# Kernel optimization log

Hardware: AMD Instinct MI355X
Metric: run time of the kernel (lower is better)

## Reference

```python
import jax, jax.numpy as jnp
import numpy as np

B, N, C, H, NUM, K = 4, 4096, 256, 512, 4, 10
GS1 = H // NUM   # feature-group size = 128
GS2 = N // NUM   # point-group size  = 1024


def _mlp2(x, w1, b1, w2, b2):
    # Linear -> ReLU -> Linear
    return jax.nn.relu(x @ w1 + b1) @ w2 + b2


def setup_inputs() -> dict:
    key = jax.random.key(0)
    ks = jax.random.split(key, 32)
    s = 0.02
    def w(i, shape):
        return jax.random.normal(ks[i], shape, dtype=jnp.float32) * s
    return {
        "features": jax.random.normal(ks[0], (B, C, N), dtype=jnp.float32),
        "xyz": jax.random.uniform(ks[1], (B, N, 3), dtype=jnp.float32),
        # fc1 / fc2 (stored [in,out] for x @ W)
        "fc1_w": w(2, (C, H)), "fc1_b": jnp.zeros((H,), jnp.float32),
        "fc2_w": w(3, (H, C)), "fc2_b": jnp.zeros((C,), jnp.float32),
        # fc_delta: Linear(3,H) -> ReLU -> Linear(H,H)
        "fd1_w": w(4, (3, H)), "fd1_b": jnp.zeros((H,), jnp.float32),
        "fd2_w": w(5, (H, H)), "fd2_b": jnp.zeros((H,), jnp.float32),
        # fc_gamma: Linear(H,H) -> ReLU -> Linear(H,H)
        "fg1_w": w(6, (H, H)), "fg1_b": jnp.zeros((H,), jnp.float32),
        "fg2_w": w(7, (H, H)), "fg2_b": jnp.zeros((H,), jnp.float32),
        # fc_gamma_2: Linear(GS1,GS1) -> ReLU -> Linear(GS1,GS1)
        "fgh1_w": w(8, (GS1, GS1)), "fgh1_b": jnp.zeros((GS1,), jnp.float32),
        "fgh2_w": w(9, (GS1, GS1)), "fgh2_b": jnp.zeros((GS1,), jnp.float32),
        # projections (no bias)
        "wqs": w(10, (H, H)), "wks": w(11, (H, H)), "wvs": w(12, (H, H)),
        "wqs2": w(13, (GS1, GS1)), "wks2": w(14, (GS1, GS1)),
    }


def reference(features, xyz, fc1_w, fc1_b, fc2_w, fc2_b, fd1_w, fd1_b, fd2_w, fd2_b,
              fg1_w, fg1_b, fg2_w, fg2_b, fgh1_w, fgh1_b, fgh2_w, fgh2_b,
              wqs, wks, wvs, wqs2, wks2):
    pre = features                                  # [B, C, N]
    x = jnp.swapaxes(features, 1, 2) @ fc1_w + fc1_b  # [B, N, H]

    # ---- attn1: feature-group subtraction attention (shared small weights per group)
    xg = x.reshape(B, N, NUM, GS1)
    q1 = jnp.einsum('bngc,cd->bngd', xg, wqs2)
    k1 = jnp.einsum('bngc,cd->bngd', xg, wks2)
    a1 = _mlp2(q1 - k1, fgh1_w, fgh1_b, fgh2_w, fgh2_b)
    a1 = jax.nn.softmax(a1 / np.sqrt(GS1).astype(np.float32), axis=1)  # softmax over points
    attn1 = a1.reshape(B, N, H)

    # ---- attn2: point-group attention. NOTE: source loop reuses stale index `i`
    # (== NUM-1) so every group is computed from the LAST point group; we replicate that.
    gf2 = x[:, (NUM - 1) * GS2:NUM * GS2, :]        # [B, GS2, H]
    q2 = gf2 @ wqs
    k2 = gf2 @ wks
    a2 = _mlp2(q2 - k2, fg1_w, fg1_b, fg2_w, fg2_b)
    a2 = jax.nn.softmax(a2 / np.sqrt(H).astype(np.float32), axis=-2)
    attn2 = jnp.tile(a2, (1, NUM, 1))               # [B, N, H]

    attn = attn1 + attn2
    v = x @ wvs                                     # [B, N, H]

    # ---- KNN positional encoding
    # square_distance
    d = (jnp.sum(xyz ** 2, -1)[:, :, None] + jnp.sum(xyz ** 2, -1)[:, None, :]
         - 2.0 * jnp.einsum('bnd,bmd->bnm', xyz, xyz))  # [B, N, N]
    knn_idx = jax.lax.top_k(-d, K)[1]               # [B, N, K] smallest distances
    knn_xyz = jax.vmap(lambda pts, idx: pts[idx])(xyz, knn_idx)  # [B, N, K, 3]
    pos_enc = _mlp2(xyz[:, :, None, :] - knn_xyz, fd1_w, fd1_b, fd2_w, fd2_b)  # [B,N,K,H]
    pos_enc = pos_enc.mean(axis=2)                  # [B, N, H]

    res = attn * (v + pos_enc)                      # einsum('bmf,bmf->bmf')
    new_features = jnp.swapaxes(res @ fc2_w + fc2_b, 1, 2) + pre  # [B, C, N]
    return (new_features, xyz)
```

## Files before the change

kernel.cpp:

```cpp
#include <hip/hip_runtime.h>
#include <cstdio>

typedef long long ll;
typedef unsigned long long ull;
typedef unsigned short ushort_t;
typedef __bf16 bf16x8 __attribute__((ext_vector_type(8)));
typedef float f32x4 __attribute__((ext_vector_type(4)));
typedef float f32x2 __attribute__((ext_vector_type(2)));

#define BB 4
#define NN 4096
#define CC 256
#define HH 512
#define GNUM 4
#define GS1 128
#define KNN 10

#define SC1 0.08838834764831845f
#define SC2 0.044194173824159216f

#define OFF_FC1T   0
#define OFF_WD2T   131072
#define OFF_FGH1T  147456
#define OFF_FGH2T  163840
#define OFF_WDT    180224
#define OFF_FG1T   442368
#define OFF_FG2T   704512
#define OFF_WVST   966656
#define OFF_FD2T   1228800
#define OFF_FC2T   1490944
#define WT_TOTAL   1622016

__device__ inline unsigned pk2(float x, float y) {
  unsigned a = __float_as_uint(x), b = __float_as_uint(y);
  a = (a + 0x7FFFu + ((a >> 16) & 1u)) >> 16;
  b = (b + 0x7FFFu + ((b >> 16) & 1u)) >> 16;
  return a | (b << 16);
}
__device__ inline ushort_t bf1(float x) {
  unsigned a = __float_as_uint(x);
  return (ushort_t)((a + 0x7FFFu + ((a >> 16) & 1u)) >> 16);
}
__device__ inline float b2f(ushort_t u) { return __uint_as_float((unsigned)u << 16); }
__device__ inline int sw16(int r) { return ((r ^ (r >> 3)) & 7) << 4; }

__device__ inline void xcd_map(int& bx, int& by, int& bz) {
  const int nx = gridDim.x, ny = gridDim.y;
  const int nwg = nx * ny * gridDim.z;
  const int bidf = blockIdx.x + nx * (blockIdx.y + ny * blockIdx.z);
  const int lid = (bidf & 7) * (nwg >> 3) + (bidf >> 3);
  bx = lid % nx;
  const int rem = lid / nx;
  by = rem % ny;
  bz = rem / ny;
}

__global__ __launch_bounds__(256) void wconv_k(
    const float* __restrict__ fc1w, const float* __restrict__ wqs2, const float* __restrict__ wks2,
    const float* __restrict__ fgh1, const float* __restrict__ fgh2,
    const float* __restrict__ wqs, const float* __restrict__ wks,
    const float* __restrict__ fg1, const float* __restrict__ fg2,
    const float* __restrict__ wvs, const float* __restrict__ fd2,
    const float* __restrict__ fc2w, ushort_t* __restrict__ WT)
{
  const int gc = blockIdx.x * 256 + threadIdx.x;
  const int e0 = gc * 8;
  if (e0 >= WT_TOTAL) return;
  const float* src = nullptr; const float* src2 = nullptr;
  int off, Kd, Nd;
  if (e0 < OFF_WD2T)        { src = fc1w;             off = OFF_FC1T;  Kd = 256; Nd = 512; }
  else if (e0 < OFF_FGH1T)  { src = wqs2; src2 = wks2; off = OFF_WD2T;  Kd = 128; Nd = 128; }
  else if (e0 < OFF_FGH2T)  { src = fgh1;             off = OFF_FGH1T; Kd = 128; Nd = 128; }
  else if (e0 < OFF_WDT)    { src = fgh2;             off = OFF_FGH2T; Kd = 128; Nd = 128; }
  else if (e0 < OFF_FG1T)   { src = wqs;  src2 = wks;  off = OFF_WDT;   Kd = 512; Nd = 512; }
  else if (e0 < OFF_FG2T)   { src = fg1;              off = OFF_FG1T;  Kd = 512; Nd = 512; }
  else if (e0 < OFF_WVST)   { src = fg2;              off = OFF_FG2T;  Kd = 512; Nd = 512; }
  else if (e0 < OFF_FD2T)   { src = wvs;              off = OFF_WVST;  Kd = 512; Nd = 512; }
  else if (e0 < OFF_FC2T)   { src = fd2;              off = OFF_FD2T;  Kd = 512; Nd = 512; }
  else                      { src = fc2w;             off = OFF_FC2T;  Kd = 512; Nd = 256; }
  const int local = e0 - off;
  const int n = local / Kd, k0 = local % Kd;
  ushort_t outv[8];
  #pragma unroll
  for (int j = 0; j < 8; ++j) {
    float v = src[(ll)(k0 + j) * Nd + n];
    if (src2) v -= src2[(ll)(k0 + j) * Nd + n];
    outv[j] = bf1(v);
  }
  *reinterpret_cast<uint4*>(WT + e0) = *reinterpret_cast<uint4*>(outv);
}

template<bool ATRANS, int EPI>
__global__ __launch_bounds__(256, 2) void mgemm_k(
    const void* __restrict__ Ain, const ushort_t* __restrict__ BT,
    const float* __restrict__ bias, void* __restrict__ CoutV,
    const float* __restrict__ pre,
    int M, int N, int K, int lda, ll strideA, ll strideC)
{
  int bx, by, z;
  xcd_map(bx, by, z);
  const int bm = by * 128;
  const int bn = bx * 128;
  __shared__ alignas(16) char smem[32768];
  char* smA = smem;
  char* smB = smem + 16384;
  const int tid = threadIdx.x;
  const int lane = tid & 63, w = tid >> 6;
  const int lr = lane & 15, lg = lane >> 4;
  const int wm = (w & 1) * 64, wn = (w >> 1) * 64;

  const ushort_t* Ab = ATRANS ? nullptr : ((const ushort_t*)Ain + (ll)z * strideA);
  const float*    Af = ATRANS ? ((const float*)Ain + (ll)z * strideA) : nullptr;

  f32x4 acc[4][4] = {};

  for (int k0 = 0; k0 < K; k0 += 64) {
    if (!ATRANS) {
      #pragma unroll
      for (int p = 0; p < 4; ++p) {
        const int i = p * 256 + tid;
        const int r = i >> 3, c8 = (i & 7) * 8;
        const uint4 v = *reinterpret_cast<const uint4*>(Ab + (ll)(bm + r) * lda + (k0 + c8));
        *reinterpret_cast<uint4*>(smA + r * 128 + ((c8 * 2) ^ sw16(r))) = v;
      }
    } else {
      #pragma unroll
      for (int p = 0; p < 2; ++p) {
        const int bb = p * 256 + tid;
        const int mb = (bb & 31) * 4, kb = (bb >> 5) * 4;
        const float4 l0 = *reinterpret_cast<const float4*>(Af + (ll)(k0 + kb + 0) * lda + (bm + mb));
        const float4 l1 = *reinterpret_cast<const float4*>(Af + (ll)(k0 + kb + 1) * lda + (bm + mb));
        const float4 l2 = *reinterpret_cast<const float4*>(Af + (ll)(k0 + kb + 2) * lda + (bm + mb));
        const float4 l3 = *reinterpret_cast<const float4*>(Af + (ll)(k0 + kb + 3) * lda + (bm + mb));
        *reinterpret_cast<uint2*>(smA + (mb + 0) * 128 + ((kb * 2) ^ sw16(mb + 0))) = make_uint2(pk2(l0.x, l1.x), pk2(l2.x, l3.x));
        *reinterpret_cast<uint2*>(smA + (mb + 1) * 128 + ((kb * 2) ^ sw16(mb + 1))) = make_uint2(pk2(l0.y, l1.y), pk2(l2.y, l3.y));
        *reinterpret_cast<uint2*>(smA + (mb + 2) * 128 + ((kb * 2) ^ sw16(mb + 2))) = make_uint2(pk2(l0.z, l1.z), pk2(l2.z, l3.z));
        *reinterpret_cast<uint2*>(smA + (mb + 3) * 128 + ((kb * 2) ^ sw16(mb + 3))) = make_uint2(pk2(l0.w, l1.w), pk2(l2.w, l3.w));
      }
    }
    #pragma unroll
    for (int p = 0; p < 4; ++p) {
      const int i = p * 256 + tid;
      const int r = i >> 3, c8 = (i & 7) * 8;
      const uint4 v = *reinterpret_cast<const uint4*>(BT + (ll)(bn + r) * K + (k0 + c8));
      *reinterpret_cast<uint4*>(smB + r * 128 + ((c8 * 2) ^ sw16(r))) = v;
    }
    __syncthreads();

    #pragma unroll
    for (int ks = 0; ks < 2; ++ks) {
      bf16x8 af[4], bfr[4];
      #pragma unroll
      for (int mi = 0; mi < 4; ++mi) {
        const int r = wm + mi * 16 + lr;
        af[mi] = *reinterpret_cast<const bf16x8*>(smA + r * 128 + ((((ks << 2) + lg) << 4) ^ sw16(r)));
      }
      #pragma unroll
      for (int ni = 0; ni < 4; ++ni) {
        const int r = wn + ni * 16 + lr;
        bfr[ni] = *reinterpret_cast<const bf16x8*>(smB + r * 128 + ((((ks << 2) + lg) << 4) ^ sw16(r)));
      }
      #pragma unroll
      for (int mi = 0; mi < 4; ++mi)
        #pragma unroll
        for (int ni = 0; ni < 4; ++ni)
          acc[mi][ni] = __builtin_amdgcn_mfma_f32_16x16x32_bf16(af[mi], bfr[ni], acc[mi][ni], 0, 0, 0);
    }
    __syncthreads();
  }

  #pragma unroll
  for (int ni = 0; ni < 4; ++ni) {
    const int col = bn + wn + ni * 16 + lr;
    const float bv = (EPI != 0) ? bias[col] : 0.f;
    #pragma unroll
    for (int mi = 0; mi < 4; ++mi) {
      const int row0 = bm + wm + mi * 16 + lg * 4;
      if (EPI == 4) {
        float* Cout = (float*)CoutV;
        const size_t o = ((size_t)z * N + col) * (size_t)M + row0;
        const float4 pv = *reinterpret_cast<const float4*>(pre + o);
        float4 r;
        r.x = acc[mi][ni][0] + bv + pv.x;
        r.y = acc[mi][ni][1] + bv + pv.y;
        r.z = acc[mi][ni][2] + bv + pv.z;
        r.w = acc[mi][ni][3] + bv + pv.w;
        *reinterpret_cast<float4*>(Cout + o) = r;
      } else {
        ushort_t* Co = (ushort_t*)CoutV + (ll)z * strideC;
        #pragma unroll
        for (int i = 0; i < 4; ++i) {
          float val = acc[mi][ni][i] + bv;
          if (EPI == 2) val = fmaxf(val, 0.f);
          Co[(ll)(row0 + i) * N + col] = bf1(val);
        }
      }
    }
  }
}

__global__ __launch_bounds__(256, 2) void gemm_vpe_k(
    const ushort_t* __restrict__ X, const ushort_t* __restrict__ HM,
    const ushort_t* __restrict__ wvT, const ushort_t* __restrict__ w2T,
    const float* __restrict__ bias, ushort_t* __restrict__ Cout)
{
  int bx, by, z;
  xcd_map(bx, by, z);
  const int bm = by * 128;
  const int bn = bx * 128;
  __shared__ alignas(16) char smem[32768];
  char* smA = smem;
  char* smB = smem + 16384;
  const int tid = threadIdx.x;
  const int lane = tid & 63, w = tid >> 6;
  const int lr = lane & 15, lg = lane >> 4;
  const int wm = (w & 1) * 64, wn = (w >> 1) * 64;

  f32x4 acc[4][4] = {};

  for (int k0 = 0; k0 < 1024; k0 += 64) {
    const ushort_t* A = (k0 < 512) ? X : HM;
    const ushort_t* BT = (k0 < 512) ? wvT : w2T;
    const int kk = k0 & 511;
    #pragma unroll
    for (int p = 0; p < 4; ++p) {
      const int i = p * 256 + tid;
      const int r = i >> 3, c8 = (i & 7) * 8;
      const uint4 v = *reinterpret_cast<const uint4*>(A + (ll)(bm + r) * 512 + (kk + c8));
      *reinterpret_cast<uint4*>(smA + r * 128 + ((c8 * 2) ^ sw16(r))) = v;
    }
    #pragma unroll
    for (int p = 0; p < 4; ++p) {
      const int i = p * 256 + tid;
      const int r = i >> 3, c8 = (i & 7) * 8;
      const uint4 v = *reinterpret_cast<const uint4*>(BT + (ll)(bn + r) * 512 + (kk + c8));
      *reinterpret_cast<uint4*>(smB + r * 128 + ((c8 * 2) ^ sw16(r))) = v;
    }
    __syncthreads();

    #pragma unroll
    for (int ks = 0; ks < 2; ++ks) {
      bf16x8 af[4], bfr[4];
      #pragma unroll
      for (int mi = 0; mi < 4; ++mi) {
        const int r = wm + mi * 16 + lr;
        af[mi] = *reinterpret_cast<const bf16x8*>(smA + r * 128 + ((((ks << 2) + lg) << 4) ^ sw16(r)));
      }
      #pragma unroll
      for (int ni = 0; ni < 4; ++ni) {
        const int r = wn + ni * 16 + lr;
        bfr[ni] = *reinterpret_cast<const bf16x8*>(smB + r * 128 + ((((ks << 2) + lg) << 4) ^ sw16(r)));
      }
      #pragma unroll
      for (int mi = 0; mi < 4; ++mi)
        #pragma unroll
        for (int ni = 0; ni < 4; ++ni)
          acc[mi][ni] = __builtin_amdgcn_mfma_f32_16x16x32_bf16(af[mi], bfr[ni], acc[mi][ni], 0, 0, 0);
    }
    __syncthreads();
  }

  #pragma unroll
  for (int ni = 0; ni < 4; ++ni) {
    const int col = bn + wn + ni * 16 + lr;
    const float bv = bias[col];
    #pragma unroll
    for (int mi = 0; mi < 4; ++mi) {
      const int row0 = bm + wm + mi * 16 + lg * 4;
      #pragma unroll
      for (int i = 0; i < 4; ++i)
        Cout[(ll)(row0 + i) * 512 + col] = bf1(acc[mi][ni][i] + bv);
    }
  }
}

__device__ __forceinline__ void gemm128(const char* smA, const char* smW, int wrow, int lr, int lg,
                                        f32x4 acc[8]) {
  #pragma unroll
  for (int ks = 0; ks < 4; ++ks) {
    const int koff = (ks * 4 + lg) * 16;
    const int ra = wrow + lr;
    const bf16x8 a = *reinterpret_cast<const bf16x8*>(smA + ra * 256 + (koff ^ sw16(ra)));
    #pragma unroll
    for (int ni = 0; ni < 8; ++ni) {
      const int rn = ni * 16 + lr;
      const bf16x8 b = *reinterpret_cast<const bf16x8*>(smW + rn * 256 + (koff ^ sw16(rn)));
      acc[ni] = __builtin_amdgcn_mfma_f32_16x16x32_bf16(a, b, acc[ni], 0, 0, 0);
    }
  }
}

__device__ __forceinline__ void stageWTb(const ushort_t* __restrict__ W, char* smW, int tid) {
  #pragma unroll
  for (int p = 0; p < 4; ++p) {
    const int i = p * 512 + tid;
    const int r = i >> 4, c8 = (i & 15) * 8;
    const uint4 v = *reinterpret_cast<const uint4*>(W + r * 128 + c8);
    *reinterpret_cast<uint4*>(smW + r * 256 + ((c8 * 2) ^ sw16(r))) = v;
  }
}

__global__ __launch_bounds__(512, 4) void fused1_k(
    const ushort_t* __restrict__ X,
    const ushort_t* __restrict__ wd2T,
    const ushort_t* __restrict__ w2T, const float* __restrict__ b2g,
    const ushort_t* __restrict__ w3T, const float* __restrict__ b3g,
    ushort_t* __restrict__ P)
{
  __shared__ alignas(16) char smT[32768];
  __shared__ alignas(16) char smW[32768];
  const int tid = threadIdx.x;
  const int lane = tid & 63, w = tid >> 6;
  const int lr = lane & 15, lg = lane >> 4;
  const int wrow = w * 16;
  const ll blockRow = (ll)blockIdx.x * 128;
  const ushort_t* Xb = X + blockRow * 128;

  float b2r[8], b3r[8];
  #pragma unroll
  for (int ni = 0; ni < 8; ++ni) { b2r[ni] = b2g[ni * 16 + lr]; b3r[ni] = b3g[ni * 16 + lr]; }

  #pragma unroll
  for (int p = 0; p < 4; ++p) {
    const int i = p * 512 + tid;
    const int r = i >> 4, c8 = (i & 15) * 8;
    const uint4 v = *reinterpret_cast<const uint4*>(Xb + (ll)r * 128 + c8);
    *reinterpret_cast<uint4*>(smT + r * 256 + ((c8 * 2) ^ sw16(r))) = v;
  }
  stageWTb(wd2T, smW, tid);
  __syncthreads();

  f32x4 acc[8];
  #pragma unroll
  for (int ni = 0; ni < 8; ++ni) acc[ni] = f32x4{0.f, 0.f, 0.f, 0.f};
  gemm128(smT, smW, wrow, lr, lg, acc);
  __syncthreads();

  #pragma unroll
  for (int ni = 0; ni < 8; ++ni)
    #pragma unroll
    for (int i = 0; i < 4; ++i) {
      const int r = wrow + lg * 4 + i;
      *reinterpret_cast<ushort_t*>(smT + r * 256 + (((ni * 16 + lr) * 2) ^ sw16(r))) = bf1(acc[ni][i]);
    }
  stageWTb(w2T, smW, tid);
  __syncthreads();

  #pragma unroll
  for (int ni = 0; ni < 8; ++ni) acc[ni] = f32x4{0.f, 0.f, 0.f, 0.f};
  gemm128(smT, smW, wrow, lr, lg, acc);
  __syncthreads();

  #pragma unroll
  for (int ni = 0; ni < 8; ++ni)
    #pragma unroll
    for (int i = 0; i < 4; ++i) {
      const int r = wrow + lg * 4 + i;
      *reinterpret_cast<ushort_t*>(smT + r * 256 + (((ni * 16 + lr) * 2) ^ sw16(r))) =
          bf1(fmaxf(acc[ni][i] + b2r[ni], 0.f));
    }
  stageWTb(w3T, smW, tid);
  __syncthreads();

  #pragma unroll
  for (int ni = 0; ni < 8; ++ni) acc[ni] = f32x4{0.f, 0.f, 0.f, 0.f};
  gemm128(smT, smW, wrow, lr, lg, acc);

  #pragma unroll
  for (int ni = 0; ni < 8; ++ni)
    #pragma unroll
    for (int i = 0; i < 4; ++i) {
      const ll r = blockRow + wrow + lg * 4 + i;
      P[r * 128 + ni * 16 + lr] = bf1(acc[ni][i] + b3r[ni]);
    }
}

__device__ inline void omax_upd(float& m, float& s, float v, float scale) {
  if (v > m) { s = s * expf((m - v) * scale) + 1.0f; m = v; }
  else       { s += expf((v - m) * scale); }
}
__device__ inline void omax_merge(float& m, float& s, float m2, float s2, float scale) {
  if (m2 > m) { s = s * expf((m - m2) * scale) + s2; m = m2; }
  else        { s += s2 * expf((m2 - m) * scale); }
}

__global__ __launch_bounds__(256) void red12_k(const ushort_t* __restrict__ P, const ushort_t* __restrict__ A2,
                                               float* __restrict__ PM1, float* __restrict__ PS1,
                                               float* __restrict__ PM2, float* __restrict__ PS2) {
  __shared__ float sm[256], ss[256];
  if (blockIdx.x < 512) {
    const int bid = blockIdx.x;
    const int b = bid >> 7, g = (bid >> 5) & 3, seg = bid & 31;
    const int d = threadIdx.x & 127, half = threadIdx.x >> 7;
    const size_t base = (size_t)b * NN * HH + g * GS1 + d;
    float m = -3.4e38f, s = 0.f;
    const int n0 = seg * 128 + half * 64;
    for (int n = n0; n < n0 + 64; ++n)
      omax_upd(m, s, b2f(P[base + (size_t)n * HH]), SC1);
    sm[threadIdx.x] = m; ss[threadIdx.x] = s;
    __syncthreads();
    if (half == 0) {
      omax_merge(m, s, sm[threadIdx.x + 128], ss[threadIdx.x + 128], SC1);
      const int c = b * HH + g * GS1 + d;
      PM1[(size_t)seg * 2048 + c] = m;
      PS1[(size_t)seg * 2048 + c] = s;
    }
  } else {
    const int bid = blockIdx.x - 512;
    const int b = bid >> 5, hb = (bid >> 3) & 3, seg = bid & 7;
    const int hl = threadIdx.x & 127, half = threadIdx.x >> 7;
    const int h = hb * 128 + hl;
    const size_t base = (size_t)b * 1024 * HH + h;
    float m = -3.4e38f, s = 0.f;
    const int r0 = seg * 128 + half * 64;
    for (int r = r0; r < r0 + 64; ++r)
      omax_upd(m, s, b2f(A2[base + (size_t)r * HH]), SC2);
    sm[threadIdx.x] = m; ss[threadIdx.x] = s;
    __syncthreads();
    if (half == 0) {
      omax_merge(m, s, sm[threadIdx.x + 128], ss[threadIdx.x + 128], SC2);
      const int c = b * HH + h;
      PM2[(size_t)seg * 2048 + c] = m;
      PS2[(size_t)seg * 2048 + c] = s;
    }
  }
}

__global__ __launch_bounds__(256) void combine12_k(const float* __restrict__ PM1, const float* __restrict__ PS1,
                                                   const float* __restrict__ PM2, const float* __restrict__ PS2,
                                                   float* __restrict__ M1, float* __restrict__ R1,
                                                   float* __restrict__ M2, float* __restrict__ R2) {
  if (blockIdx.x < 8) {
    const int c = blockIdx.x * 256 + threadIdx.x;
    float m = -3.4e38f, s = 0.f;
    for (int seg = 0; seg < 32; ++seg)
      omax_merge(m, s, PM1[(size_t)seg * 2048 + c], PS1[(size_t)seg * 2048 + c], SC1);
    M1[c] = m;
    R1[c] = 1.0f / s;
  } else {
    const int c = (blockIdx.x - 8) * 256 + threadIdx.x;
    float m = -3.4e38f, s = 0.f;
    for (int seg = 0; seg < 8; ++seg)
      omax_merge(m, s, PM2[(size_t)seg * 2048 + c], PS2[(size_t)seg * 2048 + c], SC2);
    M2[c] = m;
    R2[c] = 1.0f / s;
  }
}

__global__ __launch_bounds__(512, 8) void knn10_k(const float* __restrict__ xyz, int* __restrict__ idx) {
  const int blk = blockIdx.x;
  const int b = blk >> 8;
  const int q0 = (blk & 255) * 16;
  const float* xb = xyz + (size_t)b * NN * 3;
  const int tid = threadIdx.x;
  const int lane = tid & 63, w = tid >> 6;

  __shared__ alignas(16) float px[2048], py[2048], pz[2048], pw2[2048];
  __shared__ unsigned short candI[16][64];
  __shared__ int cnt[16];

  float qx[2], qy[2], qz[2], qn2[2];
  #pragma unroll
  for (int qq = 0; qq < 2; ++qq) {
    const int n = q0 + w * 2 + qq;
    qx[qq] = xb[n * 3]; qy[qq] = xb[n * 3 + 1]; qz[qq] = xb[n * 3 + 2];
    qn2[qq] = fmaf(qz[qq], qz[qq], fmaf(qy[qq], qy[qq], qx[qq] * qx[qq]));
  }
  if (tid < 16) cnt[tid] = 0;

  f32x2 mind[2];
  #pragma unroll
  for (int qq = 0; qq < 2; ++qq) mind[qq] = f32x2{3.4e38f, 3.4e38f};

  #pragma unroll
  for (int c = 0; c < 2; ++c) {
    __syncthreads();
    #pragma unroll
    for (int i = 0; i < 4; ++i) {
      const int p = i * 512 + tid;
      const int g = c * 2048 + p;
      const float x = xb[g * 3], y = xb[g * 3 + 1], z = xb[g * 3 + 2];
      px[p] = x; py[p] = y; pz[p] = z;
      pw2[p] = fmaf(z, z, fmaf(y, y, x * x));
    }
    __syncthreads();
    #pragma unroll 4
    for (int i = 0; i < 16; ++i) {
      const int p2 = i * 128 + lane * 2;
      const f32x2 x = *reinterpret_cast<const f32x2*>(&px[p2]);
      const f32x2 y = *reinterpret_cast<const f32x2*>(&py[p2]);
      const f32x2 z = *reinterpret_cast<const f32x2*>(&pz[p2]);
      const f32x2 pn = *reinterpret_cast<const f32x2*>(&pw2[p2]);
      #pragma unroll
      for (int qq = 0; qq < 2; ++qq) {
        f32x2 dot = x * qx[qq] + y * qy[qq] + z * qz[qq];
        const f32x2 dist = (pn + qn2[qq]) - (dot + dot);
        mind[qq].x = fminf(mind[qq].x, dist.x);
        mind[qq].y = fminf(mind[qq].y, dist.y);
      }
    }
  }

  float T[2];
  #pragma unroll
  for (int qq = 0; qq < 2; ++qq) {
    float v = fminf(mind[qq].x, mind[qq].y);
    #pragma unroll
    for (int k = 2; k <= 64; k <<= 1) {
      #pragma unroll
      for (int j = k >> 1; j > 0; j >>= 1) {
        const float o = __shfl_xor(v, j);
        const bool keepMin = (((lane & k) == 0) == ((lane & j) == 0));
        v = keepMin ? fminf(v, o) : fmaxf(v, o);
      }
    }
    T[qq] = __shfl(v, 9);
  }

  #pragma unroll
  for (int cc = 0; cc < 2; ++cc) {
    const int c = 1 - cc;
    if (c == 0) {
      __syncthreads();
      #pragma unroll
      for (int i = 0; i < 4; ++i) {
        const int p = i * 512 + tid;
        const float x = xb[p * 3], y = xb[p * 3 + 1], z = xb[p * 3 + 2];
        px[p] = x; py[p] = y; pz[p] = z;
        pw2[p] = fmaf(z, z, fmaf(y, y, x * x));
      }
      __syncthreads();
    }
    const int gbase = c * 2048;
    #pragma unroll 2
    for (int i = 0; i < 16; ++i) {
      const int p2 = i * 128 + lane * 2;
      const f32x2 x = *reinterpret_cast<const f32x2*>(&px[p2]);
      const f32x2 y = *reinterpret_cast<const f32x2*>(&py[p2]);
      const f32x2 z = *reinterpret_cast<const f32x2*>(&pz[p2]);
      const f32x2 pn = *reinterpret_cast<const f32x2*>(&pw2[p2]);
      #pragma unroll
      for (int qq = 0; qq < 2; ++qq) {
        f32x2 dot = x * qx[qq] + y * qy[qq] + z * qz[qq];
        const f32x2 dist = (pn + qn2[qq]) - (dot + dot);
        const int q = w * 2 + qq;
        if (dist.x <= T[qq]) {
          const int slot = atomicAdd(&cnt[q], 1);
          if (slot < 64) candI[q][slot] = (unsigned short)(gbase + p2);
        }
        if (dist.y <= T[qq]) {
          const int slot = atomicAdd(&cnt[q], 1);
          if (slot < 64) candI[q][slot] = (unsigned short)(gbase + p2 + 1);
        }
      }
    }
  }

  #pragma unroll
  for (int qq = 0; qq < 2; ++qq) {
    const int q = w * 2 + qq;
    const int cN = cnt[q] < 64 ? cnt[q] : 64;
    ull cv = ~0ull;
    if (lane < cN) {
      const int p = candI[q][lane];
      const float x = xb[p * 3], y = xb[p * 3 + 1], z = xb[p * 3 + 2];
      const float pn2 = fmaf(z, z, fmaf(y, y, x * x));
      const float dot = fmaf(qz[qq], z, fmaf(qy[qq], y, qx[qq] * x));
      const float dist = fmaf(-2.f, dot, qn2[qq] + pn2);
      const unsigned u = __float_as_uint(dist);
      const unsigned key = u ^ (unsigned)(((int)u >> 31) | 0x80000000);
      cv = ((ull)key << 12) | (unsigned)p;
    }
    #pragma unroll
    for (int k = 2; k <= 64; k <<= 1) {
      #pragma unroll
      for (int j = k >> 1; j > 0; j >>= 1) {
        const ull o = __shfl_xor(cv, j);
        const bool keepMin = (((lane & k) == 0) == ((lane & j) == 0));
        const bool oLess = o < cv;
        cv = (keepMin == oLess) ? o : cv;
      }
    }
    if (lane < KNN) idx[((size_t)(b * NN + q0 + q)) * KNN + lane] = (int)(cv & 0xFFFull);
  }
}

__global__ __launch_bounds__(256) void posenc_k(const float* __restrict__ xyz, const int* __restrict__ idx,
                                                const float* __restrict__ fd1w, const float* __restrict__ fd1b,
                                                ushort_t* __restrict__ hmean, float* __restrict__ outxyz) {
  const int bn = blockIdx.x;
  const int b = bn >> 12, n = bn & (NN - 1);
  const float* xb = xyz + (size_t)b * NN * 3;
  const float qx = xb[n * 3], qy = xb[n * 3 + 1], qz = xb[n * 3 + 2];
  __shared__ float dxyz[KNN][3];
  if (threadIdx.x < KNN) {
    const int m = idx[(size_t)bn * KNN + threadIdx.x];
    dxyz[threadIdx.x][0] = qx - xb[m * 3];
    dxyz[threadIdx.x][1] = qy - xb[m * 3 + 1];
    dxyz[threadIdx.x][2] = qz - xb[m * 3 + 2];
  }
  if (threadIdx.x >= 64 && threadIdx.x < 67) {
    const int c = threadIdx.x - 64;
    outxyz[(size_t)bn * 3 + c] = xb[n * 3 + c];
  }
  __syncthreads();
  for (int h = threadIdx.x; h < HH; h += 256) {
    const float w0 = fd1w[h], w1 = fd1w[HH + h], w2 = fd1w[2 * HH + h], bb = fd1b[h];
    float acc = 0.f;
    #pragma unroll
    for (int k = 0; k < KNN; ++k)
      acc += fmaxf(fmaf(dxyz[k][2], w2, fmaf(dxyz[k][1], w1, dxyz[k][0] * w0)) + bb, 0.f);
    hmean[(size_t)bn * HH + h] = bf1(acc * 0.1f);
  }
}

__global__ __launch_bounds__(256) void res_k(const ushort_t* __restrict__ P, const ushort_t* __restrict__ A2,
                                             const ushort_t* __restrict__ V,
                                             const float* __restrict__ M1, const float* __restrict__ R1,
                                             const float* __restrict__ M2, const float* __restrict__ R2,
                                             ushort_t* __restrict__ R) {
  const size_t i8 = (size_t)blockIdx.x * 256 + threadIdx.x;
  const size_t i = i8 * 8;
  const int b = (int)(i >> 21);
  const int n = (int)((i >> 9) & (NN - 1));
  const int h = (int)(i & (HH - 1));
  const int c = (b << 9) + h;
  const size_t j = (((size_t)b * 1024 + (n & 1023)) << 9) + h;
  const uint4 pu = *reinterpret_cast<const uint4*>(P + i);
  const uint4 au = *reinterpret_cast<const uint4*>(A2 + j);
  const uint4 vu = *reinterpret_cast<const uint4*>(V + i);
  float m1[8], r1[8], m2[8], r2[8];
  *reinterpret_cast<float4*>(m1) = *reinterpret_cast<const float4*>(M1 + c);
  *reinterpret_cast<float4*>(m1 + 4) = *reinterpret_cast<const float4*>(M1 + c + 4);
  *reinterpret_cast<float4*>(r1) = *reinterpret_cast<const float4*>(R1 + c);
  *reinterpret_cast<float4*>(r1 + 4) = *reinterpret_cast<const float4*>(R1 + c + 4);
  *reinterpret_cast<float4*>(m2) = *reinterpret_cast<const float4*>(M2 + c);
  *reinterpret_cast<float4*>(m2 + 4) = *reinterpret_cast<const float4*>(M2 + c + 4);
  *reinterpret_cast<float4*>(r2) = *reinterpret_cast<const float4*>(R2 + c);
  *reinterpret_cast<float4*>(r2 + 4) = *reinterpret_cast<const float4*>(R2 + c + 4);
  const unsigned* pw = reinterpret_cast<const unsigned*>(&pu);
  const unsigned* aw = reinterpret_cast<const unsigned*>(&au);
  const unsigned* vw = reinterpret_cast<const unsigned*>(&vu);
  float r[8];
  #pragma unroll
  for (int e = 0; e < 8; ++e) {
    const unsigned wsel = (e >> 1);
    const ushort_t pv = (ushort_t)((pw[wsel] >> ((e & 1) * 16)) & 0xFFFF);
    const ushort_t av = (ushort_t)((aw[wsel] >> ((e & 1) * 16)) & 0xFFFF);
    const ushort_t vv = (ushort_t)((vw[wsel] >> ((e & 1) * 16)) & 0xFFFF);
    r[e] = (expf((b2f(pv) - m1[e]) * SC1) * r1[e] + expf((b2f(av) - m2[e]) * SC2) * r2[e]) * b2f(vv);
  }
  uint4 ru;
  ru.x = pk2(r[0], r[1]);
  ru.y = pk2(r[2], r[3]);
  ru.z = pk2(r[4], r[5]);
  ru.w = pk2(r[6], r[7]);
  *reinterpret_cast<uint4*>(R + i) = ru;
}

extern "C" void kernel_launch(void* const* d_in, const int* in_sizes, int n_in,
                              void* d_out, int out_size, void* d_ws, size_t ws_size,
                              hipStream_t stream) {
  const float* features = (const float*)d_in[0];
  const float* xyz      = (const float*)d_in[1];
  const float* fc1_w    = (const float*)d_in[2];
  const float* fc1_b    = (const float*)d_in[3];
  const float* fc2_w    = (const float*)d_in[4];
  const float* fc2_b    = (const float*)d_in[5];
  const float* fd1_w    = (const float*)d_in[6];
  const float* fd1_b    = (const float*)d_in[7];
  const float* fd2_w    = (const float*)d_in[8];
  const float* fd2_b    = (const float*)d_in[9];
  const float* fg1_w    = (const float*)d_in[10];
  const float* fg1_b    = (const float*)d_in[11];
  const float* fg2_w    = (const float*)d_in[12];
  const float* fg2_b    = (const float*)d_in[13];
  const float* fgh1_w   = (const float*)d_in[14];
  const float* fgh1_b   = (const float*)d_in[15];
  const float* fgh2_w   = (const float*)d_in[16];
  const float* fgh2_b   = (const float*)d_in[17];
  const float* wqs      = (const float*)d_in[18];
  const float* wks      = (const float*)d_in[19];
  const float* wvs      = (const float*)d_in[20];
  const float* wqs2     = (const float*)d_in[21];
  const float* wks2     = (const float*)d_in[22];
  float* out = (float*)d_out;

  const size_t BNH = (size_t)BB * NN * HH;
  float* PM1 = (float*)d_ws;
  float* PS1 = PM1 + 32 * 2048;
  float* PM2 = PS1 + 32 * 2048;
  float* PS2 = PM2 + 8 * 2048;
  float* M1  = PS2 + 8 * 2048;
  float* R1  = M1 + 2048;
  float* M2  = R1 + 2048;
  float* R2  = M2 + 2048;
  int*   IDX = (int*)(R2 + 2048);
  ushort_t* WT = (ushort_t*)(IDX + (size_t)BB * NN * KNN);
  ushort_t* Xh = WT + WT_TOTAL;
  ushort_t* P  = Xh + BNH;
  ushort_t* HM = P + BNH;
  ushort_t* V  = HM + BNH;
  ushort_t* R  = V + BNH;
  ushort_t* S1 = R + BNH;
  ushort_t* S2 = S1 + (size_t)BB * 1024 * HH;
  const size_t need = ((char*)(S2 + (size_t)BB * 1024 * HH)) - (char*)d_ws;
  if (ws_size < need) {
    fprintf(stderr, "kernel_launch: ws too small: %zu < %zu\n", ws_size, need);
    return;
  }

  wconv_k<<<(WT_TOTAL / 8 + 255) / 256, 256, 0, stream>>>(
      fc1_w, wqs2, wks2, fgh1_w, fgh2_w, wqs, wks, fg1_w, fg2_w, wvs, fd2_w, fc2_w, WT);

  mgemm_k<true, 1><<<dim3(HH / 128, NN / 128, BB), 256, 0, stream>>>(
      features, WT + OFF_FC1T, fc1_b, Xh, nullptr, NN, HH, CC, NN, (ll)CC * NN, (ll)NN * HH);

  fused1_k<<<512, 512, 0, stream>>>(Xh, WT + OFF_WD2T, WT + OFF_FGH1T, fgh1_b, WT + OFF_FGH2T, fgh2_b, P);

  mgemm_k<false, 0><<<dim3(HH / 128, 1024 / 128, BB), 256, 0, stream>>>(
      Xh + (size_t)3072 * HH, WT + OFF_WDT, nullptr, S1, nullptr, 1024, HH, HH, HH, (ll)NN * HH, (ll)1024 * HH);
  mgemm_k<false, 2><<<dim3(HH / 128, BB * 1024 / 128, 1), 256, 0, stream>>>(
      S1, WT + OFF_FG1T, fg1_b, S2, nullptr, BB * 1024, HH, HH, HH, 0, 0);
  mgemm_k<false, 1><<<dim3(HH / 128, BB * 1024 / 128, 1), 256, 0, stream>>>(
      S2, WT + OFF_FG2T, fg2_b, S1, nullptr, BB * 1024, HH, HH, HH, 0, 0);

  red12_k<<<640, 256, 0, stream>>>(P, S1, PM1, PS1, PM2, PS2);
  combine12_k<<<16, 256, 0, stream>>>(PM1, PS1, PM2, PS2, M1, R1, M2, R2);

  knn10_k<<<BB * NN / 16, 512, 0, stream>>>(xyz, IDX);
  posenc_k<<<BB * NN, 256, 0, stream>>>(xyz, IDX, fd1_w, fd1_b, HM, out + (size_t)BB * CC * NN);

  gemm_vpe_k<<<dim3(HH / 128, BB * NN / 128, 1), 256, 0, stream>>>(
      Xh, HM, WT + OFF_WVST, WT + OFF_FD2T, fd2_b, V);

  res_k<<<(int)(BNH / 8 / 256), 256, 0, stream>>>(P, S1, V, M1, R1, M2, R2, R);

  mgemm_k<false, 4><<<dim3(CC / 128, NN / 128, BB), 256, 0, stream>>>(
      R, WT + OFF_FC2T, fc2_b, out, features, NN, CC, HH, HH, (ll)NN * HH, 0);
}
```

Before: 235.3 us.

## Fuse posenc into KNN kernel and attention-combine into V+pos GEMM epilogue

```diff
diff --git a/kernel.cpp b/kernel.cpp
--- a/kernel.cpp
+++ b/kernel.cpp
@@ -199,10 +199,14 @@
   }
 }
 
-__global__ __launch_bounds__(256, 2) void gemm_vpe_k(
+__global__ __launch_bounds__(256, 2) void gemm_vpe_res_k(
     const ushort_t* __restrict__ X, const ushort_t* __restrict__ HM,
     const ushort_t* __restrict__ wvT, const ushort_t* __restrict__ w2T,
-    const float* __restrict__ bias, ushort_t* __restrict__ Cout)
+    const float* __restrict__ bias,
+    const ushort_t* __restrict__ P, const ushort_t* __restrict__ A2,
+    const float* __restrict__ M1, const float* __restrict__ R1,
+    const float* __restrict__ M2, const float* __restrict__ R2,
+    ushort_t* __restrict__ Rout)
 {
   int bx, by, z;
   xcd_map(bx, by, z);
@@ -260,16 +264,26 @@
     __syncthreads();
   }
 
+  const int bb = bm >> 12;
   #pragma unroll
   for (int ni = 0; ni < 4; ++ni) {
     const int col = bn + wn + ni * 16 + lr;
     const float bv = bias[col];
+    const int c = bb * 512 + col;
+    const float m1v = M1[c], r1v = R1[c], m2v = M2[c], r2v = R2[c];
     #pragma unroll
     for (int mi = 0; mi < 4; ++mi) {
       const int row0 = bm + wm + mi * 16 + lg * 4;
       #pragma unroll
-      for (int i = 0; i < 4; ++i)
-        Cout[(ll)(row0 + i) * 512 + col] = bf1(acc[mi][ni][i] + bv);
+      for (int i = 0; i < 4; ++i) {
+        const int row = row0 + i;
+        const float v = acc[mi][ni][i] + bv;
+        const float p = b2f(P[(ll)row * 512 + col]);
+        const int rb = row & 1023;
+        const float a = b2f(A2[((ll)bb * 1024 + rb) * 512 + col]);
+        const float rr = (expf((p - m1v) * SC1) * r1v + expf((a - m2v) * SC2) * r2v) * v;
+        Rout[(ll)row * 512 + col] = bf1(rr);
+      }
     }
   }
 }
@@ -447,7 +461,9 @@
   }
 }
 
-__global__ __launch_bounds__(512, 8) void knn10_k(const float* __restrict__ xyz, int* __restrict__ idx) {
+__global__ __launch_bounds__(512, 8) void knn11_k(const float* __restrict__ xyz,
+                                                  const float* __restrict__ fd1w, const float* __restrict__ fd1b,
+                                                  ushort_t* __restrict__ HM, float* __restrict__ outxyz) {
   const int blk = blockIdx.x;
   const int b = blk >> 8;
   const int q0 = (blk & 255) * 16;
@@ -458,6 +474,7 @@
   __shared__ alignas(16) float px[2048], py[2048], pz[2048], pw2[2048];
   __shared__ unsigned short candI[16][64];
   __shared__ int cnt[16];
+  __shared__ float dx[16][KNN][3];
 
   float qx[2], qy[2], qz[2], qn2[2];
   #pragma unroll
@@ -581,81 +598,30 @@
         cv = (keepMin == oLess) ? o : cv;
       }
     }
-    if (lane < KNN) idx[((size_t)(b * NN + q0 + q)) * KNN + lane] = (int)(cv & 0xFFFull);
-  }
-}
-
-__global__ __launch_bounds__(256) void posenc_k(const float* __restrict__ xyz, const int* __restrict__ idx,
-                                                const float* __restrict__ fd1w, const float* __restrict__ fd1b,
-                                                ushort_t* __restrict__ hmean, float* __restrict__ outxyz) {
-  const int bn = blockIdx.x;
-  const int b = bn >> 12, n = bn & (NN - 1);
-  const float* xb = xyz + (size_t)b * NN * 3;
-  const float qx = xb[n * 3], qy = xb[n * 3 + 1], qz = xb[n * 3 + 2];
-  __shared__ float dxyz[KNN][3];
-  if (threadIdx.x < KNN) {
-    const int m = idx[(size_t)bn * KNN + threadIdx.x];
-    dxyz[threadIdx.x][0] = qx - xb[m * 3];
-    dxyz[threadIdx.x][1] = qy - xb[m * 3 + 1];
-    dxyz[threadIdx.x][2] = qz - xb[m * 3 + 2];
-  }
-  if (threadIdx.x >= 64 && threadIdx.x < 67) {
-    const int c = threadIdx.x - 64;
-    outxyz[(size_t)bn * 3 + c] = xb[n * 3 + c];
+    if (lane < KNN) {
+      const int p = (int)(cv & 0xFFFull);
+      dx[q][lane][0] = qx[qq] - xb[p * 3];
+      dx[q][lane][1] = qy[qq] - xb[p * 3 + 1];
+      dx[q][lane][2] = qz[qq] - xb[p * 3 + 2];
+    }
+  }
+
+  if (tid < 48) {
+    const int q = tid / 3, c = tid - q * 3;
+    outxyz[((size_t)(b * NN + q0 + q)) * 3 + c] = xb[(q0 + q) * 3 + c];
   }
   __syncthreads();
-  for (int h = threadIdx.x; h < HH; h += 256) {
-    const float w0 = fd1w[h], w1 = fd1w[HH + h], w2 = fd1w[2 * HH + h], bb = fd1b[h];
+
+  const int h = tid;
+  const float w0 = fd1w[h], w1 = fd1w[HH + h], w2 = fd1w[2 * HH + h], bbv = fd1b[h];
+  #pragma unroll
+  for (int q = 0; q < 16; ++q) {
     float acc = 0.f;
     #pragma unroll
     for (int k = 0; k < KNN; ++k)
-      acc += fmaxf(fmaf(dxyz[k][2], w2, fmaf(dxyz[k][1], w1, dxyz[k][0] * w0)) + bb, 0.f);
-    hmean[(size_t)bn * HH + h] = bf1(acc * 0.1f);
-  }
-}
-
-__global__ __launch_bounds__(256) void res_k(const ushort_t* __restrict__ P, const ushort_t* __restrict__ A2,
-                                             const ushort_t* __restrict__ V,
-                                             const float* __restrict__ M1, const float* __restrict__ R1,
-                                             const float* __restrict__ M2, const float* __restrict__ R2,
-                                             ushort_t* __restrict__ R) {
-  const size_t i8 = (size_t)blockIdx.x * 256 + threadIdx.x;
-  const size_t i = i8 * 8;
-  const int b = (int)(i >> 21);
-  const int n = (int)((i >> 9) & (NN - 1));
-  const int h = (int)(i & (HH - 1));
-  const int c = (b << 9) + h;
-  const size_t j = (((size_t)b * 1024 + (n & 1023)) << 9) + h;
-  const uint4 pu = *reinterpret_cast<const uint4*>(P + i);
-  const uint4 au = *reinterpret_cast<const uint4*>(A2 + j);
-  const uint4 vu = *reinterpret_cast<const uint4*>(V + i);
-  float m1[8], r1[8], m2[8], r2[8];
-  *reinterpret_cast<float4*>(m1) = *reinterpret_cast<const float4*>(M1 + c);
-  *reinterpret_cast<float4*>(m1 + 4) = *reinterpret_cast<const float4*>(M1 + c + 4);
-  *reinterpret_cast<float4*>(r1) = *reinterpret_cast<const float4*>(R1 + c);
-  *reinterpret_cast<float4*>(r1 + 4) = *reinterpret_cast<const float4*>(R1 + c + 4);
-  *reinterpret_cast<float4*>(m2) = *reinterpret_cast<const float4*>(M2 + c);
-  *reinterpret_cast<float4*>(m2 + 4) = *reinterpret_cast<const float4*>(M2 + c + 4);
-  *reinterpret_cast<float4*>(r2) = *reinterpret_cast<const float4*>(R2 + c);
-  *reinterpret_cast<float4*>(r2 + 4) = *reinterpret_cast<const float4*>(R2 + c + 4);
-  const unsigned* pw = reinterpret_cast<const unsigned*>(&pu);
-  const unsigned* aw = reinterpret_cast<const unsigned*>(&au);
-  const unsigned* vw = reinterpret_cast<const unsigned*>(&vu);
-  float r[8];
-  #pragma unroll
-  for (int e = 0; e < 8; ++e) {
-    const unsigned wsel = (e >> 1);
-    const ushort_t pv = (ushort_t)((pw[wsel] >> ((e & 1) * 16)) & 0xFFFF);
-    const ushort_t av = (ushort_t)((aw[wsel] >> ((e & 1) * 16)) & 0xFFFF);
-    const ushort_t vv = (ushort_t)((vw[wsel] >> ((e & 1) * 16)) & 0xFFFF);
-    r[e] = (expf((b2f(pv) - m1[e]) * SC1) * r1[e] + expf((b2f(av) - m2[e]) * SC2) * r2[e]) * b2f(vv);
-  }
-  uint4 ru;
-  ru.x = pk2(r[0], r[1]);
-  ru.y = pk2(r[2], r[3]);
-  ru.z = pk2(r[4], r[5]);
-  ru.w = pk2(r[6], r[7]);
-  *reinterpret_cast<uint4*>(R + i) = ru;
+      acc += fmaxf(fmaf(dx[q][k][2], w2, fmaf(dx[q][k][1], w1, dx[q][k][0] * w0)) + bbv, 0.f);
+    HM[((size_t)(b * NN + q0 + q)) * HH + h] = bf1(acc * 0.1f);
+  }
 }
 
 extern "C" void kernel_launch(void* const* d_in, const int* in_sizes, int n_in,
@@ -695,13 +661,11 @@
   float* R1  = M1 + 2048;
   float* M2  = R1 + 2048;
   float* R2  = M2 + 2048;
-  int*   IDX = (int*)(R2 + 2048);
-  ushort_t* WT = (ushort_t*)(IDX + (size_t)BB * NN * KNN);
+  ushort_t* WT = (ushort_t*)(R2 + 2048);
   ushort_t* Xh = WT + WT_TOTAL;
   ushort_t* P  = Xh + BNH;
   ushort_t* HM = P + BNH;
-  ushort_t* V  = HM + BNH;
-  ushort_t* R  = V + BNH;
+  ushort_t* R  = HM + BNH;
   ushort_t* S1 = R + BNH;
   ushort_t* S2 = S1 + (size_t)BB * 1024 * HH;
   const size_t need = ((char*)(S2 + (size_t)BB * 1024 * HH)) - (char*)d_ws;
@@ -728,13 +692,10 @@
   red12_k<<<640, 256, 0, stream>>>(P, S1, PM1, PS1, PM2, PS2);
   combine12_k<<<16, 256, 0, stream>>>(PM1, PS1, PM2, PS2, M1, R1, M2, R2);
 
-  knn10_k<<<BB * NN / 16, 512, 0, stream>>>(xyz, IDX);
-  posenc_k<<<BB * NN, 256, 0, stream>>>(xyz, IDX, fd1_w, fd1_b, HM, out + (size_t)BB * CC * NN);
-
-  gemm_vpe_k<<<dim3(HH / 128, BB * NN / 128, 1), 256, 0, stream>>>(
-      Xh, HM, WT + OFF_WVST, WT + OFF_FD2T, fd2_b, V);
-
-  res_k<<<(int)(BNH / 8 / 256), 256, 0, stream>>>(P, S1, V, M1, R1, M2, R2, R);
+  knn11_k<<<BB * NN / 16, 512, 0, stream>>>(xyz, fd1_w, fd1_b, HM, out + (size_t)BB * CC * NN);
+
+  gemm_vpe_res_k<<<dim3(HH / 128, BB * NN / 128, 1), 256, 0, stream>>>(
+      Xh, HM, WT + OFF_WVST, WT + OFF_FD2T, fd2_b, P, S1, M1, R1, M2, R2, R);
 
   mgemm_k<false, 4><<<dim3(CC / 128, NN / 128, BB), 256, 0, stream>>>(
       R, WT + OFF_FC2T, fc2_b, out, features, NN, CC, HH, HH, (ll)NN * HH, 0);
```

New measurement: 245.0 us. +4.1%, slower.
